# Kernel optimization log

Hardware: AMD Instinct MI355X
Metric: run time of the kernel (lower is better)

The kernel has to match this reference:

```python
import jax, jax.numpy as jnp
import numpy as np

EMBED = 400
HEADS = 4
HEAD_DIM = EMBED // HEADS  # 100
DFF = 4 * EMBED  # 1600


def setup_inputs() -> dict:
    key = jax.random.key(0)
    ks = jax.random.split(key, 12)
    s = lambda *shape: 1.0 / np.sqrt(shape[0])
    return {
        "x": jax.random.normal(ks[0], (8, 2048, EMBED), dtype=jnp.float32),
        # LayerNorm params
        "ln1_g": jnp.ones((EMBED,), jnp.float32),
        "ln1_b": jnp.zeros((EMBED,), jnp.float32),
        "ln2_g": jnp.ones((EMBED,), jnp.float32),
        "ln2_b": jnp.zeros((EMBED,), jnp.float32),
        # Per-head Q/K/V weights, stacked over heads: [H, C, D]
        "Wq": jax.random.normal(ks[1], (HEADS, EMBED, HEAD_DIM), jnp.float32) * s(EMBED),
        "Wk": jax.random.normal(ks[2], (HEADS, EMBED, HEAD_DIM), jnp.float32) * s(EMBED),
        "Wv": jax.random.normal(ks[3], (HEADS, EMBED, HEAD_DIM), jnp.float32) * s(EMBED),
        # Output projection
        "Wo": jax.random.normal(ks[4], (EMBED, EMBED), jnp.float32) * s(EMBED),
        "bo": jnp.zeros((EMBED,), jnp.float32),
        # FeedForward
        "W1": jax.random.normal(ks[5], (EMBED, DFF), jnp.float32) * s(EMBED),
        "b1": jnp.zeros((DFF,), jnp.float32),
        "W2": jax.random.normal(ks[6], (DFF, EMBED), jnp.float32) * s(DFF),
        "b2": jnp.zeros((EMBED,), jnp.float32),
    }


def _layernorm(x, g, b, eps=1e-5):
    mu = jnp.mean(x, axis=-1, keepdims=True)
    var = jnp.mean(jnp.square(x - mu), axis=-1, keepdims=True)
    return (x - mu) * jax.lax.rsqrt(var + eps) * g + b


def _block(x, ln1_g, ln1_b, ln2_g, ln2_b, Wq, Wk, Wv, Wo, bo, W1, b1, W2, b2):
    B, T, C = x.shape
    h = _layernorm(x, ln1_g, ln1_b)
    # per-head projections: [B, H, T, D]
    q = jnp.einsum("btc,hcd->bhtd", h, Wq)
    k = jnp.einsum("btc,hcd->bhtd", h, Wk)
    v = jnp.einsum("btc,hcd->bhtd", h, Wv)
    scores = jnp.einsum("bhtd,bhsd->bhts", q, k) * (1.0 / np.sqrt(HEAD_DIM))
    causal = jnp.tril(jnp.ones((T, T), dtype=bool))
    scores = jnp.where(causal, scores, -jnp.inf)
    attn = jax.nn.softmax(scores, axis=-1)
    out = jnp.einsum("bhts,bhsd->bhtd", attn, v)
    # concat heads -> [B, T, C]  (head order matches torch.concat over heads)
    out = out.transpose(0, 2, 1, 3).reshape(B, T, C)
    out = out @ Wo + bo  # dropout is identity in eval
    x = x + out
    h2 = _layernorm(x, ln2_g, ln2_b)
    ff = jax.nn.relu(h2 @ W1 + b1) @ W2 + b2  # dropout identity in eval
    return x + ff


def reference(x, ln1_g, ln1_b, ln2_g, ln2_b, Wq, Wk, Wv, Wo, bo, W1, b1, W2, b2):
    return _block(x, ln1_g, ln1_b, ln2_g, ln2_b, Wq, Wk, Wv, Wo, bo, W1, b1, W2, b2)
```

## Files before the change

### kernel.cpp

```cpp
#include <hip/hip_runtime.h>
#include <stdint.h>

#define TSEQ   2048
#define NBATCH 8
#define NHEAD  4
#define HD     100
#define EMBED  400
#define KP     416
#define QLD    1536
#define DFF    1600
#define NROWS  (NBATCH*TSEQ)

#define FLAG_RELU    1
#define FLAG_BF16OUT 2

typedef __attribute__((ext_vector_type(4))) float f32x4;
typedef __attribute__((ext_vector_type(8))) short s16x8;
typedef __attribute__((ext_vector_type(4))) unsigned short u16x4;
typedef unsigned short u16;

__device__ __forceinline__ u16 f2bf(float f) {
  union { float f; unsigned u; } v; v.f = f;
  unsigned r = v.u + 0x7FFFu + ((v.u >> 16) & 1u);
  return (u16)(r >> 16);
}

__device__ __forceinline__ void gld16(const u16* g, u16* l) {
  __builtin_amdgcn_global_load_lds(
      (const __attribute__((address_space(1))) unsigned*)g,
      (__attribute__((address_space(3))) unsigned*)l, 16, 0, 0);
}

__global__ __launch_bounds__(256) void repack_kernel(
    const float* __restrict__ Wq, const float* __restrict__ Wk, const float* __restrict__ Wv,
    const float* __restrict__ Wo, const float* __restrict__ W1, const float* __restrict__ W2,
    u16* __restrict__ wqkv, u16* __restrict__ wo, u16* __restrict__ w1, u16* __restrict__ w2)
{
  int i = blockIdx.x * 256 + threadIdx.x;
  const int n1 = 1536*KP, n2 = 512*KP, n3 = 1664*KP, n4 = 512*DFF;
  if (i < n1) {
    int n = i / KP, k = i - n*KP;
    int hh = n / 384, rem = n - hh*384;
    int w = rem >> 7, d = rem & 127;
    float v = 0.f;
    if (k < EMBED && d < HD) {
      const float* W = (w == 0) ? Wq : (w == 1) ? Wk : Wv;
      v = W[(hh*EMBED + k)*HD + d];
    }
    wqkv[i] = f2bf(v);
    return;
  }
  i -= n1;
  if (i < n2) {
    int n = i / KP, k = i - n*KP;
    float v = (n < EMBED && k < EMBED) ? Wo[k*EMBED + n] : 0.f;
    wo[i] = f2bf(v);
    return;
  }
  i -= n2;
  if (i < n3) {
    int n = i / KP, k = i - n*KP;
    float v = (n < DFF && k < EMBED) ? W1[k*DFF + n] : 0.f;
    w1[i] = f2bf(v);
    return;
  }
  i -= n3;
  if (i < n4) {
    int n = i / DFF, k = i - n*DFF;
    float v = (n < EMBED) ? W2[k*EMBED + n] : 0.f;
    w2[i] = f2bf(v);
  }
}

__global__ __launch_bounds__(256) void ln_kernel(
    const float* __restrict__ x, const float* __restrict__ gam, const float* __restrict__ bet,
    u16* __restrict__ out)
{
  int wave = threadIdx.x >> 6, lane = threadIdx.x & 63;
  int row = blockIdx.x * 4 + wave;
  const float* xr = x + row*EMBED;
  float v[7]; float s = 0.f;
  #pragma unroll
  for (int j=0;j<7;++j) { int idx = lane + j*64; v[j] = (idx < EMBED) ? xr[idx] : 0.f; s += v[j]; }
  #pragma unroll
  for (int off=1; off<64; off<<=1) s += __shfl_xor(s, off, 64);
  float mu = s * (1.f/EMBED);
  float q = 0.f;
  #pragma unroll
  for (int j=0;j<7;++j) { int idx = lane + j*64; if (idx < EMBED) { float d = v[j]-mu; q += d*d; } }
  #pragma unroll
  for (int off=1; off<64; off<<=1) q += __shfl_xor(q, off, 64);
  float rstd = rsqrtf(q * (1.f/EMBED) + 1e-5f);
  u16* orow = out + row*KP;
  #pragma unroll
  for (int j=0;j<7;++j) {
    int idx = lane + j*64;
    if (idx < KP) {
      float o = (idx < EMBED) ? (v[j]-mu)*rstd*gam[idx] + bet[idx] : 0.f;
      orow[idx] = f2bf(o);
    }
  }
}

__global__ __launch_bounds__(256) void gemm_bf16(
    const u16* __restrict__ A, int lda,
    const u16* __restrict__ Bt, int ldb,
    void* __restrict__ Cout, int ldc,
    const float* __restrict__ bias,
    const float* __restrict__ resid, int ldres,
    int N, int ksteps, int flags)
{
  __shared__ u16 As[128*32];
  __shared__ u16 Bs[128*32];
  const int tid  = threadIdx.x;
  const int lane = tid & 63, wave = tid >> 6;
  const int wm = wave >> 1, wn = wave & 1;
  const int r15 = lane & 15, g = lane >> 4;
  const int brow = blockIdx.x * 128;
  const int bcol = blockIdx.y * 128;

  f32x4 acc[4][4] = {};
  const int c0 = wave*128 + lane;

  for (int ks = 0; ks < ksteps; ++ks) {
    #pragma unroll
    for (int i=0;i<2;++i) {
      int c = c0 + i*64;
      int r = c >> 2, kc = c & 3;
      gld16(A  + (brow + r)*lda + ks*32 + kc*8, As + c*8);
      gld16(Bt + (bcol + r)*ldb + ks*32 + kc*8, Bs + c*8);
    }
    __syncthreads();
    s16x8 af[4], bq[4];
    #pragma unroll
    for (int mi=0;mi<4;++mi)
      af[mi] = *(const s16x8*)(As + (wm*64 + mi*16 + r15)*32 + g*8);
    #pragma unroll
    for (int ni=0;ni<4;++ni)
      bq[ni] = *(const s16x8*)(Bs + (wn*64 + ni*16 + r15)*32 + g*8);
    #pragma unroll
    for (int mi=0;mi<4;++mi)
      #pragma unroll
      for (int ni=0;ni<4;++ni)
        acc[mi][ni] = __builtin_amdgcn_mfma_f32_16x16x32_bf16(af[mi], bq[ni], acc[mi][ni], 0, 0, 0);
    __syncthreads();
  }

  #pragma unroll
  for (int ni=0;ni<4;++ni) {
    const int col = bcol + wn*64 + ni*16 + r15;
    if (col >= N) continue;
    const float bv = bias ? bias[col] : 0.f;
    #pragma unroll
    for (int mi=0;mi<4;++mi) {
      #pragma unroll
      for (int e=0;e<4;++e) {
        const int row = brow + wm*64 + mi*16 + g*4 + e;
        float v = acc[mi][ni][e] + bv;
        if (flags & FLAG_RELU) v = fmaxf(v, 0.f);
        if (resid) v += resid[row*ldres + col];
        if (flags & FLAG_BF16OUT) ((u16*)Cout)[row*ldc + col] = f2bf(v);
        else                      ((float*)Cout)[row*ldc + col] = v;
      }
    }
  }
}

#define VS 68
__global__ __launch_bounds__(512, 2) void attn_kernel(
    const u16* __restrict__ qkv, u16* __restrict__ aout)
{
  const int p  = blockIdx.x;
  const int bh = blockIdx.y;
  const int b = bh >> 2, h = bh & 3;
  const int tid = threadIdx.x;
  const int lane = tid & 63, wave = tid >> 6;
  const int r15 = lane & 15, g = lane >> 4;

  __shared__ u16 Ks[2][64*128];
  __shared__ u16 Vt[112*VS];
  __shared__ u16 Ps[8*16*VS];

  const int base = (b*TSEQ)*QLD + h*384;
  const int q0A = p*128;
  const int q0B = (15-p)*128;
  const int ntB = 2*(15-p) + 2;

  auto stageK = [&](int buf, int kj) {
    #pragma unroll
    for (int i=0;i<2;++i) {
      int c = (wave*2 + i)*64 + lane;
      int r = c >> 4, pos = c & 15;
      int dc = pos ^ (r & 7);
      gld16(qkv + base + 128 + (kj*64 + r)*QLD + dc*8, &Ks[buf][c*8]);
    }
  };

  s16x8 vv[2];
  auto loadV = [&](int kj) {
    #pragma unroll
    for (int i=0;i<2;++i) {
      int c = tid + i*512;
      if (c < 896) {
        int kv = c & 63, dc2 = c >> 6;
        vv[i] = *(const s16x8*)(qkv + base + 256 + (kj*64 + kv)*QLD + dc2*8);
      }
    }
  };
  auto writeV = [&]() {
    #pragma unroll
    for (int i=0;i<2;++i) {
      int c = tid + i*512;
      if (c < 896) {
        int kv = c & 63, dc2 = c >> 6;
        #pragma unroll
        for (int e=0;e<8;++e) Vt[(dc2*8+e)*VS + kv] = (u16)vv[i][e];
      }
    }
  };

  stageK(0, 0);
  loadV(0);
  s16x8 qfA[4], qfB[4];
  #pragma unroll
  for (int ks=0;ks<4;++ks) {
    qfA[ks] = *(const s16x8*)(qkv + base + (q0A + wave*16 + r15)*QLD + ks*32 + g*8);
    qfB[ks] = *(const s16x8*)(qkv + base + (q0B + wave*16 + r15)*QLD + ks*32 + g*8);
  }
  __syncthreads();
  writeV();
  __syncthreads();

  f32x4 accA[7] = {}, accB[7] = {};
  float lA[4] = {}, lB[4] = {};

  u16* myP = Ps + wave*16*VS;

  auto tileCompute = [&](const s16x8* qf, f32x4* acc, float* lsum, int q0t,
                         int kj, int cur) {
    f32x4 sacc[4] = {};
    #pragma unroll
    for (int ni=0;ni<4;++ni) {
      #pragma unroll
      for (int ks=0;ks<4;++ks) {
        int row = ni*16 + r15;
        int pos = (ks*4 + g) ^ (row & 7);
        s16x8 kf = *(const s16x8*)(&Ks[cur][row*128 + pos*8]);
        sacc[ni] = __builtin_amdgcn_mfma_f32_16x16x32_bf16(qf[ks], kf, sacc[ni], 0, 0, 0);
      }
    }
    const int qrow_g = q0t + wave*16 + g*4;
    #pragma unroll
    for (int ni=0;ni<4;++ni) {
      int kvg = kj*64 + ni*16 + r15;
      #pragma unroll
      for (int e=0;e<4;++e) {
        float pe = (kvg > qrow_g + e) ? 0.f : __expf(sacc[ni][e] * 0.1f);
        sacc[ni][e] = pe;
        lsum[e] += pe;
      }
    }
    #pragma unroll
    for (int ni=0;ni<4;++ni)
      #pragma unroll
      for (int e=0;e<4;++e)
        myP[(g*4+e)*VS + ni*16 + r15] = f2bf(sacc[ni][e]);
    s16x8 pa[2];
    #pragma unroll
    for (int ks2=0;ks2<2;++ks2)
      pa[ks2] = *(const s16x8*)(myP + r15*VS + ks2*32 + g*8);
    #pragma unroll
    for (int ni=0;ni<7;++ni) {
      #pragma unroll
      for (int ks2=0;ks2<2;++ks2) {
        s16x8 vf = *(const s16x8*)(Vt + (ni*16 + r15)*VS + ks2*32 + g*8);
        acc[ni] = __builtin_amdgcn_mfma_f32_16x16x32_bf16(pa[ks2], vf, acc[ni], 0, 0, 0);
      }
    }
  };

  for (int kj = 0; kj < ntB; ++kj) {
    const int cur = kj & 1;
    if (kj+1 < ntB) { stageK(cur^1, kj+1); loadV(kj+1); }
    if (kj*64 <= q0A + wave*16 + 15) tileCompute(qfA, accA, lA, q0A, kj, cur);
    if (kj*64 <= q0B + wave*16 + 15) tileCompute(qfB, accB, lB, q0B, kj, cur);
    __syncthreads();
    if (kj+1 < ntB) { writeV(); __syncthreads(); }
  }

  #pragma unroll
  for (int e=0;e<4;++e) {
    float a = lA[e], bb = lB[e];
    a += __shfl_xor(a, 1, 64);  bb += __shfl_xor(bb, 1, 64);
    a += __shfl_xor(a, 2, 64);  bb += __shfl_xor(bb, 2, 64);
    a += __shfl_xor(a, 4, 64);  bb += __shfl_xor(bb, 4, 64);
    a += __shfl_xor(a, 8, 64);  bb += __shfl_xor(bb, 8, 64);
    lA[e] = a; lB[e] = bb;
  }
  #pragma unroll
  for (int ni=0;ni<7;++ni) {
    int d = ni*16 + r15;
    if (d < HD) {
      #pragma unroll
      for (int e=0;e<4;++e) {
        int rowA = b*TSEQ + q0A + wave*16 + g*4 + e;
        int rowB = b*TSEQ + q0B + wave*16 + g*4 + e;
        aout[rowA*KP + h*HD + d] = f2bf(accA[ni][e] / lA[e]);
        aout[rowB*KP + h*HD + d] = f2bf(accB[ni][e] / lB[e]);
      }
    }
  }
  if (h == 0) {
    int r = tid >> 2, c4 = tid & 3;
    int rowA = b*TSEQ + q0A + r;
    int rowB = b*TSEQ + q0B + r;
    *(u16x4*)(aout + rowA*KP + EMBED + c4*4) = (u16x4){0,0,0,0};
    *(u16x4*)(aout + rowB*KP + EMBED + c4*4) = (u16x4){0,0,0,0};
  }
}

extern "C" void kernel_launch(void* const* d_in, const int* in_sizes, int n_in,
                              void* d_out, int out_size, void* d_ws, size_t ws_size,
                              hipStream_t stream)
{
  const float* x    = (const float*)d_in[0];
  const float* ln1g = (const float*)d_in[1];
  const float* ln1b = (const float*)d_in[2];
  const float* ln2g = (const float*)d_in[3];
  const float* ln2b = (const float*)d_in[4];
  const float* Wq   = (const float*)d_in[5];
  const float* Wk   = (const float*)d_in[6];
  const float* Wv   = (const float*)d_in[7];
  const float* Wo   = (const float*)d_in[8];
  const float* bo   = (const float*)d_in[9];
  const float* W1   = (const float*)d_in[10];
  const float* b1   = (const float*)d_in[11];
  const float* W2   = (const float*)d_in[12];
  const float* b2   = (const float*)d_in[13];

  u16* wsu = (u16*)d_ws;
  u16* wqkv_t = wsu;
  u16* wo_t   = wsu + 638976;
  u16* w1_t   = wsu + 851968;
  u16* w2_t   = wsu + 1544192;
  char* wsb = (char*)d_ws;
  u16* h_bf  = (u16*)(wsb + 4726784);
  u16* qkv   = (u16*)(wsb + 18358272);
  u16* attn  = (u16*)(wsb + 68689920);
  u16* ff    = h_bf;
  float* x2  = (float*)d_out;

  repack_kernel<<<(2363392 + 255)/256, 256, 0, stream>>>(Wq, Wk, Wv, Wo, W1, W2,
                                                         wqkv_t, wo_t, w1_t, w2_t);
  ln_kernel<<<NROWS/4, 256, 0, stream>>>(x, ln1g, ln1b, h_bf);
  gemm_bf16<<<dim3(NROWS/128, 12), 256, 0, stream>>>(h_bf, KP, wqkv_t, KP, qkv, QLD,
      nullptr, nullptr, 0, QLD, KP/32, FLAG_BF16OUT);
  attn_kernel<<<dim3(8, NBATCH*NHEAD), 512, 0, stream>>>(qkv, attn);
  gemm_bf16<<<dim3(NROWS/128, 4), 256, 0, stream>>>(attn, KP, wo_t, KP, x2, EMBED,
      bo, x, EMBED, EMBED, KP/32, 0);
  ln_kernel<<<NROWS/4, 256, 0, stream>>>(x2, ln2g, ln2b, attn );
  gemm_bf16<<<dim3(NROWS/128, 13), 256, 0, stream>>>(attn, KP, w1_t, KP, ff, DFF,
      b1, nullptr, 0, DFF, KP/32, FLAG_BF16OUT | FLAG_RELU);
  gemm_bf16<<<dim3(NROWS/128, 4), 256, 0, stream>>>(ff, DFF, w2_t, DFF, (float*)d_out, EMBED,
      b2, x2, EMBED, EMBED, DFF/32, 0);
}
```

Before: 406.4 us.

## Double-buffer GEMM LDS loads and widen tiles to 128x256 with 512 threads

Measured after the change: 394.2 us. 1.03x faster.

```diff
diff --git a/kernel.cpp b/kernel.cpp
--- a/kernel.cpp
+++ b/kernel.cpp
@@ -37,7 +37,7 @@
     u16* __restrict__ wqkv, u16* __restrict__ wo, u16* __restrict__ w1, u16* __restrict__ w2)
 {
   int i = blockIdx.x * 256 + threadIdx.x;
-  const int n1 = 1536*KP, n2 = 512*KP, n3 = 1664*KP, n4 = 512*DFF;
+  const int n1 = 1536*KP, n2 = 512*KP, n3 = 1792*KP, n4 = 512*DFF;
   if (i < n1) {
     int n = i / KP, k = i - n*KP;
     int hh = n / 384, rem = n - hh*384;
@@ -102,42 +102,51 @@
   }
 }
 
-__global__ __launch_bounds__(256) void gemm_bf16(
+template<int KSTEPS>
+__global__ __launch_bounds__(512, 4) void gemm_bf16(
     const u16* __restrict__ A, int lda,
     const u16* __restrict__ Bt, int ldb,
     void* __restrict__ Cout, int ldc,
     const float* __restrict__ bias,
     const float* __restrict__ resid, int ldres,
-    int N, int ksteps, int flags)
-{
-  __shared__ u16 As[128*32];
-  __shared__ u16 Bs[128*32];
+    int N, int flags)
+{
+  __shared__ u16 As[2][128*32];
+  __shared__ u16 Bs[2][256*32];
   const int tid  = threadIdx.x;
   const int lane = tid & 63, wave = tid >> 6;
-  const int wm = wave >> 1, wn = wave & 1;
+  const int wm = wave >> 2, wn = wave & 3;
   const int r15 = lane & 15, g = lane >> 4;
   const int brow = blockIdx.x * 128;
-  const int bcol = blockIdx.y * 128;
+  const int bcol = blockIdx.y * 256;
 
   f32x4 acc[4][4] = {};
-  const int c0 = wave*128 + lane;
-
-  for (int ks = 0; ks < ksteps; ++ks) {
+
+  auto stage = [&](int buf, int ks) {
+    { int c = tid;
+      int r = c >> 2, kc = c & 3;
+      gld16(A + (brow + r)*lda + ks*32 + kc*8, &As[buf][c*8]); }
     #pragma unroll
     for (int i=0;i<2;++i) {
-      int c = c0 + i*64;
+      int c = tid + i*512;
       int r = c >> 2, kc = c & 3;
-      gld16(A  + (brow + r)*lda + ks*32 + kc*8, As + c*8);
-      gld16(Bt + (bcol + r)*ldb + ks*32 + kc*8, Bs + c*8);
-    }
-    __syncthreads();
+      gld16(Bt + (bcol + r)*ldb + ks*32 + kc*8, &Bs[buf][c*8]);
+    }
+  };
+
+  stage(0, 0);
+  __syncthreads();
+
+  for (int ks = 0; ks < KSTEPS; ++ks) {
+    const int cur = ks & 1;
+    if (ks+1 < KSTEPS) stage(cur^1, ks+1);
     s16x8 af[4], bq[4];
     #pragma unroll
     for (int mi=0;mi<4;++mi)
-      af[mi] = *(const s16x8*)(As + (wm*64 + mi*16 + r15)*32 + g*8);
+      af[mi] = *(const s16x8*)(&As[cur][(wm*64 + mi*16 + r15)*32 + g*8]);
     #pragma unroll
     for (int ni=0;ni<4;++ni)
-      bq[ni] = *(const s16x8*)(Bs + (wn*64 + ni*16 + r15)*32 + g*8);
+      bq[ni] = *(const s16x8*)(&Bs[cur][(wn*64 + ni*16 + r15)*32 + g*8]);
     #pragma unroll
     for (int mi=0;mi<4;++mi)
       #pragma unroll
@@ -342,25 +351,25 @@
   u16* wqkv_t = wsu;
   u16* wo_t   = wsu + 638976;
   u16* w1_t   = wsu + 851968;
-  u16* w2_t   = wsu + 1544192;
+  u16* w2_t   = wsu + 1597440;
   char* wsb = (char*)d_ws;
-  u16* h_bf  = (u16*)(wsb + 4726784);
-  u16* qkv   = (u16*)(wsb + 18358272);
-  u16* attn  = (u16*)(wsb + 68689920);
+  u16* h_bf  = (u16*)(wsb + 4833280);
+  u16* qkv   = (u16*)(wsb + 18464768);
+  u16* attn  = (u16*)(wsb + 68796416);
   u16* ff    = h_bf;
   float* x2  = (float*)d_out;
 
-  repack_kernel<<<(2363392 + 255)/256, 256, 0, stream>>>(Wq, Wk, Wv, Wo, W1, W2,
+  repack_kernel<<<(2416640 + 255)/256, 256, 0, stream>>>(Wq, Wk, Wv, Wo, W1, W2,
                                                          wqkv_t, wo_t, w1_t, w2_t);
   ln_kernel<<<NROWS/4, 256, 0, stream>>>(x, ln1g, ln1b, h_bf);
-  gemm_bf16<<<dim3(NROWS/128, 12), 256, 0, stream>>>(h_bf, KP, wqkv_t, KP, qkv, QLD,
-      nullptr, nullptr, 0, QLD, KP/32, FLAG_BF16OUT);
+  gemm_bf16<13><<<dim3(NROWS/128, 6), 512, 0, stream>>>(h_bf, KP, wqkv_t, KP, qkv, QLD,
+      nullptr, nullptr, 0, QLD, FLAG_BF16OUT);
   attn_kernel<<<dim3(8, NBATCH*NHEAD), 512, 0, stream>>>(qkv, attn);
-  gemm_bf16<<<dim3(NROWS/128, 4), 256, 0, stream>>>(attn, KP, wo_t, KP, x2, EMBED,
-      bo, x, EMBED, EMBED, KP/32, 0);
+  gemm_bf16<13><<<dim3(NROWS/128, 2), 512, 0, stream>>>(attn, KP, wo_t, KP, x2, EMBED,
+      bo, x, EMBED, EMBED, 0);
   ln_kernel<<<NROWS/4, 256, 0, stream>>>(x2, ln2g, ln2b, attn );
-  gemm_bf16<<<dim3(NROWS/128, 13), 256, 0, stream>>>(attn, KP, w1_t, KP, ff, DFF,
-      b1, nullptr, 0, DFF, KP/32, FLAG_BF16OUT | FLAG_RELU);
-  gemm_bf16<<<dim3(NROWS/128, 4), 256, 0, stream>>>(ff, DFF, w2_t, DFF, (float*)d_out, EMBED,
-      b2, x2, EMBED, EMBED, DFF/32, 0);
-}
+  gemm_bf16<13><<<dim3(NROWS/128, 7), 512, 0, stream>>>(attn, KP, w1_t, KP, ff, DFF,
+      b1, nullptr, 0, DFF, FLAG_BF16OUT | FLAG_RELU);
+  gemm_bf16<50><<<dim3(NROWS/128, 2), 512, 0, stream>>>(ff, DFF, w2_t, DFF, (float*)d_out, EMBED,
+      b2, x2, EMBED, EMBED, 0);
+}
```
